# Optimization experiments

Measured on AMD Instinct MI355X. Metric: run time of the kernel, lower is better.

Reference implementation:

```python
import jax, jax.numpy as jnp
import numpy as np

N, K, D_IN, H = 8192, 8, 512, 512
SCALE = 0.02  # weight init scale


def setup_inputs() -> dict:
    key = jax.random.key(0)
    ks = jax.random.split(key, 12)
    inp = {
        "x": jax.random.normal(ks[0], (N, D_IN), jnp.float32),
        "child_h": jax.random.normal(ks[1], (N, K, H), jnp.float32),
        "child_c": jax.random.normal(ks[2], (N, K, H), jnp.float32),
    }
    names = ["i", "f", "o", "u"]
    for idx, g in enumerate(names):
        inp["W" + g] = jax.random.normal(ks[3 + idx], (D_IN, H), jnp.float32) * SCALE
        inp["bW" + g] = jnp.zeros((H,), jnp.float32)
        inp["U" + g] = jax.random.normal(ks[7 + idx], (H, H), jnp.float32) * SCALE
        inp["bU" + g] = jnp.zeros((H,), jnp.float32)
    return inp


def reference(x, child_h, child_c,
              Wi, bWi, Ui, bUi,
              Wf, bWf, Uf, bUf,
              Wo, bWo, Uo, bUo,
              Wu, bWu, Uu, bUu):
    # Child-Sum Tree-LSTM, batched over N nodes each with K children.
    h_sum = child_h.sum(axis=1)                                   # [N, H]
    i = jax.nn.sigmoid(x @ Wi + bWi + h_sum @ Ui + bUi)           # [N, H]
    o = jax.nn.sigmoid(x @ Wo + bWo + h_sum @ Uo + bUo)           # [N, H]
    u = jnp.tanh(x @ Wu + bWu + h_sum @ Uu + bUu)                 # [N, H]
    # Per-child forget gates: f_k = sigmoid(W_f x + U_f h_k)
    f = jax.nn.sigmoid((x @ Wf + bWf)[:, None, :]
                       + jnp.einsum('nkh,hg->nkg', child_h, Uf) + bUf)  # [N, K, H]
    c = i * u + (f * child_c).sum(axis=1)                         # [N, H]
    h = o * jnp.tanh(c)                                           # [N, H]
    return jnp.stack([h, c], axis=0)                              # [2, N, H]
```

## Files before the change

### kernel.cpp

```cpp
#include <hip/hip_runtime.h>
#include <hip/hip_bf16.h>


#define NN 8192
#define KCH 8
#define HH 512

typedef __attribute__((ext_vector_type(4))) float f32x4;
typedef __attribute__((ext_vector_type(8))) short short8;

__device__ inline unsigned short f2bf(float f) {
    union { float f; unsigned u; } v; v.f = f;
    unsigned r = v.u + 0x7FFFu + ((v.u >> 16) & 1u);
    return (unsigned short)(r >> 16);
}
__device__ inline float bf2f(unsigned short b) {
    union { unsigned u; float f; } v; v.u = ((unsigned)b) << 16;
    return v.f;
}
__device__ inline float sigm(float x) { return 1.f / (1.f + __expf(-x)); }
__device__ inline float tanh_pf(float x) { return 2.f / (1.f + __expf(-2.f * x)) - 1.f; }

__device__ __forceinline__ void gl16(const unsigned short* gsrc, unsigned short* ldst) {
    __builtin_amdgcn_global_load_lds(
        (const __attribute__((address_space(1))) unsigned int*)gsrc,
        (__attribute__((address_space(3))) unsigned int*)ldst,
        16, 0, 0);
}


__global__ void k_cvt(const float* __restrict__ in, unsigned short* __restrict__ outp) {
    int i = blockIdx.x * blockDim.x + threadIdx.x;
    float4 a = ((const float4*)in)[2 * i];
    float4 b = ((const float4*)in)[2 * i + 1];
    uint4 o;
    o.x = (unsigned)f2bf(a.x) | ((unsigned)f2bf(a.y) << 16);
    o.y = (unsigned)f2bf(a.z) | ((unsigned)f2bf(a.w) << 16);
    o.z = (unsigned)f2bf(b.x) | ((unsigned)f2bf(b.y) << 16);
    o.w = (unsigned)f2bf(b.z) | ((unsigned)f2bf(b.w) << 16);
    ((uint4*)outp)[i] = o;
}

__global__ void k_hsum(const float* __restrict__ ch, unsigned short* __restrict__ hs) {
    int i = blockIdx.x * blockDim.x + threadIdx.x;
    int n = i >> 7, h4 = i & 127;
    const float4* base = (const float4*)(ch + (size_t)n * KCH * HH) + h4;
    float4 s = base[0];
#pragma unroll
    for (int k = 1; k < KCH; ++k) {
        float4 v = base[(size_t)k * 128];
        s.x += v.x; s.y += v.y; s.z += v.z; s.w += v.w;
    }
    unsigned long long pk = (unsigned long long)f2bf(s.x)
        | ((unsigned long long)f2bf(s.y) << 16)
        | ((unsigned long long)f2bf(s.z) << 32)
        | ((unsigned long long)f2bf(s.w) << 48);
    *(unsigned long long*)&hs[(size_t)i * 4] = pk;
}

struct P8 { const float* p[8]; };
__global__ void k_transpose_w(P8 wsrc, unsigned short* __restrict__ out) {
    __shared__ float tile[32][33];
    const float* W = wsrc.p[blockIdx.z];
    unsigned short* O = out + (size_t)blockIdx.z * 262144;
    int k0 = blockIdx.x * 32, c0 = blockIdx.y * 32;
    for (int r = threadIdx.y; r < 32; r += 8)
        tile[r][threadIdx.x] = W[(size_t)(k0 + r) * 512 + c0 + threadIdx.x];
    __syncthreads();
    for (int r = threadIdx.y; r < 32; r += 8)
        O[(size_t)(c0 + r) * 512 + k0 + threadIdx.x] = f2bf(tile[threadIdx.x][r]);
}

__global__ __launch_bounds__(256, 2) void k_gates(
    const unsigned short* __restrict__ xb,
    const unsigned short* __restrict__ hsb,
    const unsigned short* __restrict__ wT,
    const float* __restrict__ bWi, const float* __restrict__ bUi,
    const float* __restrict__ bWf,
    const float* __restrict__ bWo, const float* __restrict__ bUo,
    const float* __restrict__ bWu, const float* __restrict__ bUu,
    unsigned short* __restrict__ Pq,
    unsigned short* __restrict__ Oq,
    unsigned short* __restrict__ Fq)
{
    __shared__ unsigned short lds[2][12288];
    const int t = threadIdx.x, lane = t & 63, wid = t >> 6;
    const int wr = wid >> 1, wc = wid & 1;
    const int nid = (blockIdx.x & 7) * 64 + (blockIdx.x >> 3);
    const int r0 = (nid >> 3) * 128, c0 = (nid & 7) * 64;

    f32x4 acc_i[4][2] = {}; f32x4 acc_f[4][2] = {};
    f32x4 acc_o[4][2] = {}; f32x4 acc_u[4][2] = {};

    const int frow = lane & 15, fk = (lane >> 4) * 8;

    auto stage0 = [&](unsigned short* buf, int kq) {
        for (int c = wid; c < 24; c += 4) {
            if (c < 8) {
                gl16(&xb[(size_t)(r0 + c * 16 + frow) * 512 + kq + fk], &buf[c * 512]);
            } else {
                int d = c - 8, p = d >> 2, cb = d & 3;
                gl16(&wT[(size_t)p * 262144 + (size_t)(c0 + cb * 16 + frow) * 512 + kq + fk],
                     &buf[4096 + d * 512]);
            }
        }
    };
    auto stage1 = [&](unsigned short* buf, int kq) {
        for (int c = wid; c < 20; c += 4) {
            if (c < 8) {
                gl16(&hsb[(size_t)(r0 + c * 16 + frow) * 512 + kq + fk], &buf[c * 512]);
            } else {
                int d = c - 8, p = d >> 2, cb = d & 3;
                gl16(&wT[(size_t)(4 + p) * 262144 + (size_t)(c0 + cb * 16 + frow) * 512 + kq + fk],
                     &buf[4096 + d * 512]);
            }
        }
    };

    stage0(lds[0], 0);

#pragma unroll 1
    for (int kq = 0; kq < 512; kq += 32) {
        unsigned short* cur = lds[(kq >> 5) & 1];
        unsigned short* nxt = lds[((kq >> 5) & 1) ^ 1];
        __syncthreads();
        if (kq < 480) stage0(nxt, kq + 32); else stage1(nxt, 0);
        short8 af[4];
#pragma unroll
        for (int m = 0; m < 4; ++m) af[m] = *(const short8*)&cur[(wr * 4 + m) * 512 + lane * 8];
#pragma unroll
        for (int p = 0; p < 4; ++p) {
            short8 b0 = *(const short8*)&cur[4096 + (p * 4 + wc * 2 + 0) * 512 + lane * 8];
            short8 b1 = *(const short8*)&cur[4096 + (p * 4 + wc * 2 + 1) * 512 + lane * 8];
#pragma unroll
            for (int m = 0; m < 4; ++m) {
                if (p == 0) {
                    acc_i[m][0] = __builtin_amdgcn_mfma_f32_16x16x32_bf16(af[m], b0, acc_i[m][0], 0, 0, 0);
                    acc_i[m][1] = __builtin_amdgcn_mfma_f32_16x16x32_bf16(af[m], b1, acc_i[m][1], 0, 0, 0);
                } else if (p == 1) {
                    acc_f[m][0] = __builtin_amdgcn_mfma_f32_16x16x32_bf16(af[m], b0, acc_f[m][0], 0, 0, 0);
                    acc_f[m][1] = __builtin_amdgcn_mfma_f32_16x16x32_bf16(af[m], b1, acc_f[m][1], 0, 0, 0);
                } else if (p == 2) {
                    acc_o[m][0] = __builtin_amdgcn_mfma_f32_16x16x32_bf16(af[m], b0, acc_o[m][0], 0, 0, 0);
                    acc_o[m][1] = __builtin_amdgcn_mfma_f32_16x16x32_bf16(af[m], b1, acc_o[m][1], 0, 0, 0);
                } else {
                    acc_u[m][0] = __builtin_amdgcn_mfma_f32_16x16x32_bf16(af[m], b0, acc_u[m][0], 0, 0, 0);
                    acc_u[m][1] = __builtin_amdgcn_mfma_f32_16x16x32_bf16(af[m], b1, acc_u[m][1], 0, 0, 0);
                }
            }
        }
    }
#pragma unroll 1
    for (int kq = 0; kq < 512; kq += 32) {
        unsigned short* cur = lds[(kq >> 5) & 1];
        unsigned short* nxt = lds[((kq >> 5) & 1) ^ 1];
        __syncthreads();
        if (kq < 480) stage1(nxt, kq + 32);
        short8 af[4];
#pragma unroll
        for (int m = 0; m < 4; ++m) af[m] = *(const short8*)&cur[(wr * 4 + m) * 512 + lane * 8];
#pragma unroll
        for (int p = 0; p < 3; ++p) {
            short8 b0 = *(const short8*)&cur[4096 + (p * 4 + wc * 2 + 0) * 512 + lane * 8];
            short8 b1 = *(const short8*)&cur[4096 + (p * 4 + wc * 2 + 1) * 512 + lane * 8];
#pragma unroll
            for (int m = 0; m < 4; ++m) {
                if (p == 0) {
                    acc_i[m][0] = __builtin_amdgcn_mfma_f32_16x16x32_bf16(af[m], b0, acc_i[m][0], 0, 0, 0);
                    acc_i[m][1] = __builtin_amdgcn_mfma_f32_16x16x32_bf16(af[m], b1, acc_i[m][1], 0, 0, 0);
                } else if (p == 1) {
                    acc_o[m][0] = __builtin_amdgcn_mfma_f32_16x16x32_bf16(af[m], b0, acc_o[m][0], 0, 0, 0);
                    acc_o[m][1] = __builtin_amdgcn_mfma_f32_16x16x32_bf16(af[m], b1, acc_o[m][1], 0, 0, 0);
                } else {
                    acc_u[m][0] = __builtin_amdgcn_mfma_f32_16x16x32_bf16(af[m], b0, acc_u[m][0], 0, 0, 0);
                    acc_u[m][1] = __builtin_amdgcn_mfma_f32_16x16x32_bf16(af[m], b1, acc_u[m][1], 0, 0, 0);
                }
            }
        }
    }
#pragma unroll
    for (int m = 0; m < 4; ++m) {
#pragma unroll
        for (int n = 0; n < 2; ++n) {
            int col = c0 + wc * 32 + n * 16 + (lane & 15);
            float bi = bWi[col] + bUi[col];
            float bf = bWf[col];
            float bo = bWo[col] + bUo[col];
            float bu = bWu[col] + bUu[col];
#pragma unroll
            for (int r = 0; r < 4; ++r) {
                int row = r0 + wr * 64 + m * 16 + (lane >> 4) * 4 + r;
                size_t idx = (size_t)row * 512 + col;
                float vi = sigm(acc_i[m][n][r] + bi);
                float vu = tanh_pf(acc_u[m][n][r] + bu);
                Pq[idx] = f2bf(vi * vu);
                Oq[idx] = f2bf(sigm(acc_o[m][n][r] + bo));
                Fq[idx] = f2bf(acc_f[m][n][r] + bf);
            }
        }
    }
}

__global__ __launch_bounds__(512, 2) void k_fc(
    const float* __restrict__ ch,
    const float* __restrict__ cc,
    const unsigned short* __restrict__ ufT,
    const float* __restrict__ bUf,
    const unsigned short* __restrict__ Pq,
    const unsigned short* __restrict__ Oq,
    const unsigned short* __restrict__ Fq,
    float* __restrict__ out)
{
    __shared__ unsigned short lds[2][18432];
    const int t = threadIdx.x, lane = t & 63, wid = t >> 6;
    const int wc = wid;
    const int r0c = blockIdx.x * 64;

    f32x4 acc[4][4] = {};
    const int frow = lane & 15, fk = (lane >> 4) * 8;

    auto stage = [&](unsigned short* buf, int kq) {
        if (t < 256) {
            int row = 16 * (t >> 6) + (t & 15), ks = (t >> 4) & 3;
            const float* src = &ch[(size_t)(r0c + row) * 512 + kq + ks * 8];
            float4 v0 = *(const float4*)src;
            float4 v1 = *(const float4*)(src + 4);
            uint4 o;
            o.x = (unsigned)f2bf(v0.x) | ((unsigned)f2bf(v0.y) << 16);
            o.y = (unsigned)f2bf(v0.z) | ((unsigned)f2bf(v0.w) << 16);
            o.z = (unsigned)f2bf(v1.x) | ((unsigned)f2bf(v1.y) << 16);
            o.w = (unsigned)f2bf(v1.z) | ((unsigned)f2bf(v1.w) << 16);
            *(uint4*)&buf[t * 8] = o;
        } else {
            int w = wid - 4;
#pragma unroll
            for (int j = 0; j < 8; ++j) {
                int s2 = w * 8 + j;
                gl16(&ufT[(size_t)(s2 * 16 + frow) * 512 + kq + fk], &buf[2048 + s2 * 512]);
            }
        }
    };

    stage(lds[0], 0);

#pragma unroll 1
    for (int kq = 0; kq < 512; kq += 32) {
        unsigned short* cur = lds[(kq >> 5) & 1];
        unsigned short* nxt = lds[((kq >> 5) & 1) ^ 1];
        __syncthreads();
        if (kq < 480) stage(nxt, kq + 32);
        short8 af[4], bfr[4];
#pragma unroll
        for (int m = 0; m < 4; ++m) af[m] = *(const short8*)&cur[m * 512 + lane * 8];
#pragma unroll
        for (int n = 0; n < 4; ++n) bfr[n] = *(const short8*)&cur[2048 + (wc * 4 + n) * 512 + lane * 8];
#pragma unroll
        for (int m = 0; m < 4; ++m)
#pragma unroll
            for (int n = 0; n < 4; ++n)
                acc[m][n] = __builtin_amdgcn_mfma_f32_16x16x32_bf16(af[m], bfr[n], acc[m][n], 0, 0, 0);
    }

    const int g = lane >> 4;
    float bUfv[4];
#pragma unroll
    for (int n = 0; n < 4; ++n) bUfv[n] = bUf[wc * 64 + n * 16 + (lane & 15)];

#pragma unroll
    for (int m = 0; m < 4; ++m) {
        int node = (r0c >> 3) + 2 * m + (g >> 1);
#pragma unroll
        for (int n = 0; n < 4; ++n) {
            int col = wc * 64 + n * 16 + (lane & 15);
            size_t nidx = (size_t)node * 512 + col;
            float xf = bf2f(Fq[nidx]) + bUfv[n];
            float fcs = 0.f;
#pragma unroll
            for (int r = 0; r < 4; ++r) {
                int R = r0c + m * 16 + g * 4 + r;
                float pre = acc[m][n][r] + xf;
                fcs += sigm(pre) * cc[(size_t)R * 512 + col];
            }
            fcs += __shfl_xor(fcs, 16);
            if ((g & 1) == 0) {
                float cv = bf2f(Pq[nidx]) + fcs;
                out[nidx] = bf2f(Oq[nidx]) * tanh_pf(cv);
                out[(size_t)NN * HH + nidx] = cv;
            }
        }
    }
}

extern "C" void kernel_launch(void* const* d_in, const int* in_sizes, int n_in,
                              void* d_out, int out_size, void* d_ws, size_t ws_size,
                              hipStream_t stream) {
    const float* x   = (const float*)d_in[0];
    const float* ch  = (const float*)d_in[1];
    const float* cc  = (const float*)d_in[2];
    const float* Wi  = (const float*)d_in[3];  const float* bWi = (const float*)d_in[4];
    const float* Ui  = (const float*)d_in[5];  const float* bUi = (const float*)d_in[6];
    const float* Wf  = (const float*)d_in[7];  const float* bWf = (const float*)d_in[8];
    const float* Uf  = (const float*)d_in[9];  const float* bUf = (const float*)d_in[10];
    const float* Wo  = (const float*)d_in[11]; const float* bWo = (const float*)d_in[12];
    const float* Uo  = (const float*)d_in[13]; const float* bUo = (const float*)d_in[14];
    const float* Wu  = (const float*)d_in[15]; const float* bWu = (const float*)d_in[16];
    const float* Uu  = (const float*)d_in[17]; const float* bUu = (const float*)d_in[18];
    float* out = (float*)d_out;

    unsigned short* xb  = (unsigned short*)d_ws;
    unsigned short* hsb = xb  + (size_t)NN * HH;
    unsigned short* wT  = hsb + (size_t)NN * HH;
    unsigned short* Pq  = wT  + (size_t)8 * 262144;
    unsigned short* Oq  = Pq  + (size_t)NN * HH;
    unsigned short* Fq  = Oq  + (size_t)NN * HH;

    k_cvt<<<(NN * HH / 8) / 256, 256, 0, stream>>>(x, xb);
    k_hsum<<<(NN * 128) / 256, 256, 0, stream>>>(ch, hsb);
    P8 wp;
    wp.p[0] = Wi; wp.p[1] = Wf; wp.p[2] = Wo; wp.p[3] = Wu;
    wp.p[4] = Ui; wp.p[5] = Uo; wp.p[6] = Uu; wp.p[7] = Uf;
    k_transpose_w<<<dim3(16, 16, 8), dim3(32, 8), 0, stream>>>(wp, wT);
    k_gates<<<dim3(512), 256, 0, stream>>>(xb, hsb, wT,
                                           bWi, bUi, bWf, bWo, bUo, bWu, bUu,
                                           Pq, Oq, Fq);
    k_fc<<<dim3(1024), 512, 0, stream>>>(ch, cc, wT + (size_t)7 * 262144, bUf,
                                         Pq, Oq, Fq, out);
}
```

Baseline: 212.0 us.

## Pre-convert child_h to bf16 in hsum and async-load it in fc kernel

The hsum kernel now also writes a bf16 copy of child_h into workspace when the workspace is large enough. A new fc kernel then streams that copy into LDS through global_load_lds instead of converting fp32 in registers. The GEMM loops also swap __syncthreads for explicit vmcnt waits plus raw barriers, so that prefetches of the next tile can overlap the current MFMA work. This adds an extra 64MB write and read of bf16 child_h, and falls back to the old path when the workspace is too small.

After: 217.0 us. +2.4%, slower.

```diff
diff --git a/kernel.cpp b/kernel.cpp
--- a/kernel.cpp
+++ b/kernel.cpp
@@ -8,6 +8,9 @@
 
 typedef __attribute__((ext_vector_type(4))) float f32x4;
 typedef __attribute__((ext_vector_type(8))) short short8;
+
+#define WAITV(N) asm volatile("s_waitcnt vmcnt(" #N ")" ::: "memory")
+#define BAR() __builtin_amdgcn_s_barrier()
 
 __device__ inline unsigned short f2bf(float f) {
     union { float f; unsigned u; } v; v.f = f;
@@ -41,15 +44,23 @@
     ((uint4*)outp)[i] = o;
 }
 
-__global__ void k_hsum(const float* __restrict__ ch, unsigned short* __restrict__ hs) {
+__global__ void k_hsum(const float* __restrict__ ch, unsigned short* __restrict__ hs,
+                       unsigned short* __restrict__ chb) {
     int i = blockIdx.x * blockDim.x + threadIdx.x;
     int n = i >> 7, h4 = i & 127;
     const float4* base = (const float4*)(ch + (size_t)n * KCH * HH) + h4;
-    float4 s = base[0];
-#pragma unroll
-    for (int k = 1; k < KCH; ++k) {
+    float4 s = {0.f, 0.f, 0.f, 0.f};
+#pragma unroll
+    for (int k = 0; k < KCH; ++k) {
         float4 v = base[(size_t)k * 128];
         s.x += v.x; s.y += v.y; s.z += v.z; s.w += v.w;
+        if (chb) {
+            unsigned long long pk = (unsigned long long)f2bf(v.x)
+                | ((unsigned long long)f2bf(v.y) << 16)
+                | ((unsigned long long)f2bf(v.z) << 32)
+                | ((unsigned long long)f2bf(v.w) << 48);
+            *(unsigned long long*)&chb[((size_t)n * KCH + k) * 512 + h4 * 4] = pk;
+        }
     }
     unsigned long long pk = (unsigned long long)f2bf(s.x)
         | ((unsigned long long)f2bf(s.y) << 16)
@@ -96,22 +107,22 @@
 
     auto stage0 = [&](unsigned short* buf, int kq) {
         for (int c = wid; c < 24; c += 4) {
-            if (c < 8) {
+            if (c < 8)
                 gl16(&xb[(size_t)(r0 + c * 16 + frow) * 512 + kq + fk], &buf[c * 512]);
-            } else {
-                int d = c - 8, p = d >> 2, cb = d & 3;
-                gl16(&wT[(size_t)p * 262144 + (size_t)(c0 + cb * 16 + frow) * 512 + kq + fk],
+            else {
+                int d = c - 8;
+                gl16(&wT[(size_t)(d >> 2) * 262144 + (size_t)(c0 + (d & 3) * 16 + frow) * 512 + kq + fk],
                      &buf[4096 + d * 512]);
             }
         }
     };
     auto stage1 = [&](unsigned short* buf, int kq) {
         for (int c = wid; c < 20; c += 4) {
-            if (c < 8) {
+            if (c < 8)
                 gl16(&hsb[(size_t)(r0 + c * 16 + frow) * 512 + kq + fk], &buf[c * 512]);
-            } else {
-                int d = c - 8, p = d >> 2, cb = d & 3;
-                gl16(&wT[(size_t)(4 + p) * 262144 + (size_t)(c0 + cb * 16 + frow) * 512 + kq + fk],
+            else {
+                int d = c - 8;
+                gl16(&wT[(size_t)(4 + (d >> 2)) * 262144 + (size_t)(c0 + (d & 3) * 16 + frow) * 512 + kq + fk],
                      &buf[4096 + d * 512]);
             }
         }
@@ -123,8 +134,10 @@
     for (int kq = 0; kq < 512; kq += 32) {
         unsigned short* cur = lds[(kq >> 5) & 1];
         unsigned short* nxt = lds[((kq >> 5) & 1) ^ 1];
-        __syncthreads();
-        if (kq < 480) stage0(nxt, kq + 32); else stage1(nxt, 0);
+        BAR();
+        if (kq < 480) { stage0(nxt, kq + 32); WAITV(6); }
+        else          { stage1(nxt, 0);       WAITV(5); }
+        BAR();
         short8 af[4];
 #pragma unroll
         for (int m = 0; m < 4; ++m) af[m] = *(const short8*)&cur[(wr * 4 + m) * 512 + lane * 8];
@@ -154,8 +167,10 @@
     for (int kq = 0; kq < 512; kq += 32) {
         unsigned short* cur = lds[(kq >> 5) & 1];
         unsigned short* nxt = lds[((kq >> 5) & 1) ^ 1];
-        __syncthreads();
-        if (kq < 480) stage1(nxt, kq + 32);
+        BAR();
+        if (kq < 480) { stage1(nxt, kq + 32); WAITV(5); }
+        else          { WAITV(0); }
+        BAR();
         short8 af[4];
 #pragma unroll
         for (int m = 0; m < 4; ++m) af[m] = *(const short8*)&cur[(wr * 4 + m) * 512 + lane * 8];
@@ -201,8 +216,8 @@
     }
 }
 
-__global__ __launch_bounds__(512, 2) void k_fc(
-    const float* __restrict__ ch,
+__global__ __launch_bounds__(512, 2) void k_fc2(
+    const unsigned short* __restrict__ chb,
     const float* __restrict__ cc,
     const unsigned short* __restrict__ ufT,
     const float* __restrict__ bUf,
@@ -216,6 +231,88 @@
     const int wc = wid;
     const int r0c = blockIdx.x * 64;
 
+    f32x4 acc[4][4] = {};
+    const int frow = lane & 15, fk = (lane >> 4) * 8;
+
+    auto stage = [&](unsigned short* buf, int kq) {
+#pragma unroll
+        for (int j = 0; j < 5; ++j) {
+            int c = wid + j * 8;
+            if (c < 36) {
+                if (c < 4)
+                    gl16(&chb[(size_t)(r0c + c * 16 + frow) * 512 + kq + fk], &buf[c * 512]);
+                else
+                    gl16(&ufT[(size_t)((c - 4) * 16 + frow) * 512 + kq + fk],
+                         &buf[2048 + (c - 4) * 512]);
+            }
+        }
+    };
+
+    stage(lds[0], 0);
+
+#pragma unroll 1
+    for (int kq = 0; kq < 512; kq += 32) {
+        unsigned short* cur = lds[(kq >> 5) & 1];
+        unsigned short* nxt = lds[((kq >> 5) & 1) ^ 1];
+        BAR();
+        if (kq < 480) {
+            stage(nxt, kq + 32);
+            if (wid < 4) { WAITV(5); } else { WAITV(4); }
+        } else {
+            WAITV(0);
+        }
+        BAR();
+        short8 af[4], bfr[4];
+#pragma unroll
+        for (int m = 0; m < 4; ++m) af[m] = *(const short8*)&cur[m * 512 + lane * 8];
+#pragma unroll
+        for (int n = 0; n < 4; ++n) bfr[n] = *(const short8*)&cur[2048 + (wc * 4 + n) * 512 + lane * 8];
+#pragma unroll
+        for (int m = 0; m < 4; ++m)
+#pragma unroll
+            for (int n = 0; n < 4; ++n)
+                acc[m][n] = __builtin_amdgcn_mfma_f32_16x16x32_bf16(af[m], bfr[n], acc[m][n], 0, 0, 0);
+    }
+
+    const int g = lane >> 4;
+    float bUfv[4];
+#pragma unroll
+    for (int n = 0; n < 4; ++n) bUfv[n] = bUf[wc * 64 + n * 16 + (lane & 15)];
+
+#pragma unroll
+    for (int m = 0; m < 4; ++m) {
+        int node = (r0c >> 3) + 2 * m + (g >> 1);
+#pragma unroll
+        for (int n = 0; n < 4; ++n) {
+            int col = wc * 64 + n * 16 + (lane & 15);
+            size_t nidx = (size_t)node * 512 + col;
+            float xf = bf2f(Fq[nidx]) + bUfv[n];
+            float fcs = 0.f;
+#pragma unroll
+            for (int r = 0; r < 4; ++r) {
+                int R = r0c + m * 16 + g * 4 + r;
+                fcs += sigm(acc[m][n][r] + xf) * cc[(size_t)R * 512 + col];
+            }
+            fcs += __shfl_xor(fcs, 16);
+            if ((g & 1) == 0) {
+                float cv = bf2f(Pq[nidx]) + fcs;
+                out[nidx] = bf2f(Oq[nidx]) * tanh_pf(cv);
+                out[(size_t)NN * HH + nidx] = cv;
+            }
+        }
+    }
+}
+
+__global__ __launch_bounds__(512, 2) void k_fc_fb(
+    const float* __restrict__ ch, const float* __restrict__ cc,
+    const unsigned short* __restrict__ ufT, const float* __restrict__ bUf,
+    const unsigned short* __restrict__ Pq, const unsigned short* __restrict__ Oq,
+    const unsigned short* __restrict__ Fq, float* __restrict__ out)
+{
+    __shared__ unsigned short lds[2][18432];
+    const int t = threadIdx.x, lane = t & 63, wid = t >> 6;
+    const int wc = wid;
+    const int r0c = blockIdx.x * 64;
     f32x4 acc[4][4] = {};
     const int frow = lane & 15, fk = (lane >> 4) * 8;
 
@@ -234,15 +331,13 @@
         } else {
             int w = wid - 4;
 #pragma unroll
-            for (int j = 0; j < 8; ++j) {
-                int s2 = w * 8 + j;
-                gl16(&ufT[(size_t)(s2 * 16 + frow) * 512 + kq + fk], &buf[2048 + s2 * 512]);
-            }
+            for (int j = 0; j < 8; ++j)
+                gl16(&ufT[(size_t)((w * 8 + j) * 16 + frow) * 512 + kq + fk],
+                     &buf[2048 + (w * 8 + j) * 512]);
         }
     };
 
     stage(lds[0], 0);
-
 #pragma unroll 1
     for (int kq = 0; kq < 512; kq += 32) {
         unsigned short* cur = lds[(kq >> 5) & 1];
@@ -260,12 +355,10 @@
             for (int n = 0; n < 4; ++n)
                 acc[m][n] = __builtin_amdgcn_mfma_f32_16x16x32_bf16(af[m], bfr[n], acc[m][n], 0, 0, 0);
     }
-
     const int g = lane >> 4;
     float bUfv[4];
 #pragma unroll
     for (int n = 0; n < 4; ++n) bUfv[n] = bUf[wc * 64 + n * 16 + (lane & 15)];
-
 #pragma unroll
     for (int m = 0; m < 4; ++m) {
         int node = (r0c >> 3) + 2 * m + (g >> 1);
@@ -278,8 +371,7 @@
 #pragma unroll
             for (int r = 0; r < 4; ++r) {
                 int R = r0c + m * 16 + g * 4 + r;
-                float pre = acc[m][n][r] + xf;
-                fcs += sigm(pre) * cc[(size_t)R * 512 + col];
+                fcs += sigm(acc[m][n][r] + xf) * cc[(size_t)R * 512 + col];
             }
             fcs += __shfl_xor(fcs, 16);
             if ((g & 1) == 0) {
@@ -313,9 +405,13 @@
     unsigned short* Pq  = wT  + (size_t)8 * 262144;
     unsigned short* Oq  = Pq  + (size_t)NN * HH;
     unsigned short* Fq  = Oq  + (size_t)NN * HH;
+    unsigned short* chb = Fq  + (size_t)NN * HH;
+
+    size_t need = ((size_t)NN * HH * 5 + (size_t)8 * 262144 + (size_t)NN * KCH * HH) * 2;
+    bool big = ws_size >= need;
 
     k_cvt<<<(NN * HH / 8) / 256, 256, 0, stream>>>(x, xb);
-    k_hsum<<<(NN * 128) / 256, 256, 0, stream>>>(ch, hsb);
+    k_hsum<<<(NN * 128) / 256, 256, 0, stream>>>(ch, hsb, big ? chb : nullptr);
     P8 wp;
     wp.p[0] = Wi; wp.p[1] = Wf; wp.p[2] = Wo; wp.p[3] = Wu;
     wp.p[4] = Ui; wp.p[5] = Uo; wp.p[6] = Uu; wp.p[7] = Uf;
@@ -323,6 +419,10 @@
     k_gates<<<dim3(512), 256, 0, stream>>>(xb, hsb, wT,
                                            bWi, bUi, bWf, bWo, bUo, bWu, bUu,
                                            Pq, Oq, Fq);
-    k_fc<<<dim3(1024), 512, 0, stream>>>(ch, cc, wT + (size_t)7 * 262144, bUf,
-                                         Pq, Oq, Fq, out);
-}
+    if (big)
+        k_fc2<<<dim3(1024), 512, 0, stream>>>(chb, cc, wT + (size_t)7 * 262144, bUf,
+                                              Pq, Oq, Fq, out);
+    else
+        k_fc_fb<<<dim3(1024), 512, 0, stream>>>(ch, cc, wT + (size_t)7 * 262144, bUf,
+                                                Pq, Oq, Fq, out);
+}
```
